# Kernel tuning notes

Measured on AMD Instinct MI355X. Metric: run time of the kernel, lower is better.

Reference implementation:

```python
import jax, jax.numpy as jnp
import numpy as np

NC = 1
LAMBDA_BOX = 0.05
LAMBDA_OBJ = 1.0
LAMBDA_CLS = 0.5

# yolov5s pixel-space anchors (already stride-scaled): [n_scales=3, A=3, 2]
_ANCHORS = np.array([[[10, 13], [16, 30], [33, 23]],
                     [[30, 61], [62, 45], [59, 119]],
                     [[116, 90], [156, 198], [373, 326]]], dtype=np.float32)

B, N = 64, 32
GRIDS = [160, 80, 40]  # 1280px input, strides 8/16/32


def setup_inputs() -> dict:
    key = jax.random.key(0)
    k0, k1, k2, kb = jax.random.split(key, 4)
    A = _ANCHORS.shape[1]
    preds = {}
    for i, (k, g) in enumerate(zip((k0, k1, k2), GRIDS)):
        preds[f"pred{i}"] = jax.random.normal(k, (B, A * (NC + 5), g, g), dtype=jnp.float32)
    # normalized cxcywh boxes, kept strictly inside (0,1) so gi<W, gj<H and w,h>0
    boxes = jax.random.uniform(kb, (B, N, 4), minval=0.02, maxval=0.98, dtype=jnp.float32)
    labels = jnp.zeros((B, N), dtype=jnp.int32)  # nc=1 -> all class 0
    scaled_anchors = jnp.asarray(_ANCHORS)
    return {**preds, "boxes": boxes, "labels": labels, "scaled_anchors": scaled_anchors}


def _scale_loss(pred, boxes, anchor_grid, nc):
    # pred: [B, A*(nc+5), H, W]; boxes: [B, N, 4] normalized cxcywh; anchor_grid: [A, 2]
    Bc, _, H, W = pred.shape
    A = anchor_grid.shape[0]
    Nc = boxes.shape[1]
    p = pred.reshape(Bc, A, nc + 5, H, W).transpose(0, 1, 3, 4, 2)  # [B,A,H,W,nc+5]

    scale = jnp.array([W, H, W, H], dtype=pred.dtype)
    bx = boxes * scale                                   # grid-space cxcywh [B,N,4]
    gx, gy, gw, gh = bx[..., 0], bx[..., 1], bx[..., 2], bx[..., 3]
    gi = gx.astype(jnp.int32)                            # int() truncation (boxes > 0)
    gj = gy.astype(jnp.int32)

    # anchor matching: min(ratio, 1/ratio) product, argmax over A
    r = anchor_grid[None, None, :, :] / bx[..., None, 2:4]   # [B,N,A,2]
    ious = jnp.minimum(r, 1.0 / r).prod(-1)                  # [B,N,A]
    best = jnp.argmax(ious, axis=-1)                         # [B,N]

    bi = jnp.broadcast_to(jnp.arange(Bc)[:, None], (Bc, Nc))
    idx = (bi, best, gj, gi)
    aw = anchor_grid[best, 0]
    ah = anchor_grid[best, 1]

    z = jnp.zeros((Bc, A, H, W), dtype=pred.dtype)
    obj = jnp.zeros((Bc, A, H, W), dtype=bool).at[idx].set(True)
    tx = z.at[idx].set(gx - gi.astype(pred.dtype))
    ty = z.at[idx].set(gy - gj.astype(pred.dtype))
    tw = z.at[idx].set(jnp.log(gw / aw + 1e-16))
    th = z.at[idx].set(jnp.log(gh / ah + 1e-16))

    objf = obj.astype(pred.dtype)
    n_pos = objf.sum()
    n_neg = (1.0 - objf).sum()

    # sum of 4 per-component MSE means == combined squared-error sum / n_pos
    sq = ((p[..., 0] - tx) ** 2 + (p[..., 1] - ty) ** 2
          + (p[..., 2] - tw) ** 2 + (p[..., 3] - th) ** 2)
    loss_box = (sq * objf).sum() / n_pos

    po = p[..., 4]
    # BCEWithLogits: target 1 -> softplus(-x); target 0 -> softplus(x)
    loss_obj = ((jax.nn.softplus(-po) * objf).sum() / n_pos
                + (jax.nn.softplus(po) * (1.0 - objf)).sum() / n_neg)
    return loss_box, loss_obj


def reference(pred0, pred1, pred2, boxes, labels, scaled_anchors):
    del labels  # nc == 1 -> original skips the classification loss
    loss_box = 0.0
    loss_obj = 0.0
    for i, pred in enumerate((pred0, pred1, pred2)):
        lb, lo = _scale_loss(pred, boxes, scaled_anchors[i], NC)
        loss_box = loss_box + lb
        loss_obj = loss_obj + lo
    return LAMBDA_BOX * loss_box + LAMBDA_OBJ * loss_obj
```

## Files before the change

kernel.cpp:

```cpp
#include <hip/hip_runtime.h>
#include <math.h>

#define NSCALES 3
#define BATCH 64
#define NBOX 32

#define CELLS0 4915200
#define CELLS1 1228800
#define CELLS2 307200

#define NB0 1200
#define NB1 300
#define NB2 75

struct Accum {
    double box_sum[3];
    double pos_sum[3];
    double neg_corr[3];
    double neg_total[3];
    int n_pos[3];
    int pad;
};

__device__ __forceinline__ float softplusf(float x) {
    return fmaxf(x, 0.0f) + log1pf(expf(-fabsf(x)));
}

__global__ __launch_bounds__(64) void targets_kernel(
    const float* __restrict__ pred0, const float* __restrict__ pred1,
    const float* __restrict__ pred2, const float* __restrict__ boxes,
    const float* __restrict__ anchors, Accum* __restrict__ acc)
{
    const int bs = blockIdx.x;
    const int s  = bs / BATCH;
    const int b  = bs % BATCH;
    const int G  = (s == 0) ? 160 : (s == 1 ? 80 : 40);
    const float* __restrict__ pred = (s == 0) ? pred0 : (s == 1 ? pred1 : pred2);
    const int HW = G * G;
    const int t  = threadIdx.x;

    __shared__ int keys[NBOX];

    float sq = 0.0f, posv = 0.0f, negc = 0.0f;
    int cnt = 0;

    int key = -1;
    float gx = 0.f, gy = 0.f, gw = 1.f, gh = 1.f;
    int gi = 0, gj = 0, best = 0;

    if (t < NBOX) {
        const float4 bx = ((const float4*)boxes)[b * NBOX + t];
        const float fG = (float)G;
        gx = bx.x * fG; gy = bx.y * fG; gw = bx.z * fG; gh = bx.w * fG;
        float bestm = -1.0f;
        #pragma unroll
        for (int a = 0; a < 3; ++a) {
            float aw = anchors[s * 6 + a * 2 + 0];
            float ah = anchors[s * 6 + a * 2 + 1];
            float rw = aw / gw, rh = ah / gh;
            float m = fminf(rw, 1.0f / rw) * fminf(rh, 1.0f / rh);
            if (m > bestm) { bestm = m; best = a; }
        }
        gi = (int)gx;
        gj = (int)gy;
        key = (best * G + gj) * G + gi;
        keys[t] = key;
    }
    __syncthreads();

    if (t < NBOX) {
        bool winner = true;
        for (int u = t + 1; u < NBOX; ++u)
            if (keys[u] == key) winner = false;
        if (winner) {
            float aw = anchors[s * 6 + best * 2 + 0];
            float ah = anchors[s * 6 + best * 2 + 1];
            float tx = gx - (float)gi;
            float ty = gy - (float)gj;
            float tw = logf(gw / aw + 1e-16f);
            float th = logf(gh / ah + 1e-16f);
            size_t base = (size_t)((b * 3 + best) * 6) * (size_t)HW + (size_t)(gj * G + gi);
            float px = pred[base + (size_t)0 * HW];
            float py = pred[base + (size_t)1 * HW];
            float pw = pred[base + (size_t)2 * HW];
            float ph = pred[base + (size_t)3 * HW];
            float po = pred[base + (size_t)4 * HW];
            float dx = px - tx, dy = py - ty, dw = pw - tw, dh = ph - th;
            sq   = dx * dx + dy * dy + dw * dw + dh * dh;
            posv = softplusf(-po);
            negc = softplusf(po);
            cnt  = 1;
        }
    }

    #pragma unroll
    for (int off = 32; off; off >>= 1) {
        sq   += __shfl_down(sq, off);
        posv += __shfl_down(posv, off);
        negc += __shfl_down(negc, off);
        cnt  += __shfl_down(cnt, off);
    }
    if (t == 0) {
        atomicAdd(&acc->box_sum[s],  (double)sq);
        atomicAdd(&acc->pos_sum[s],  (double)posv);
        atomicAdd(&acc->neg_corr[s], (double)negc);
        atomicAdd(&acc->n_pos[s],    cnt);
    }
}

__global__ __launch_bounds__(256) void obj_kernel(
    const float4* __restrict__ p0, const float4* __restrict__ p1,
    const float4* __restrict__ p2, Accum* __restrict__ acc)
{
    const int blk = blockIdx.x;
    int s, HW4, base4;
    const float4* __restrict__ p;
    if (blk < NB0)            { s = 0; p = p0; HW4 = 6400; base4 = blk * 1024; }
    else if (blk < NB0 + NB1) { s = 1; p = p1; HW4 = 1600; base4 = (blk - NB0) * 1024; }
    else                      { s = 2; p = p2; HW4 = 400;  base4 = (blk - NB0 - NB1) * 1024; }

    float sum = 0.0f;
    #pragma unroll
    for (int k = 0; k < 4; ++k) {
        int i4    = base4 + k * 256 + threadIdx.x;
        int plane = i4 / HW4;
        int off4  = i4 - plane * HW4;
        float4 v  = p[(size_t)(plane * 6 + 4) * HW4 + off4];
        sum += softplusf(v.x) + softplusf(v.y) + softplusf(v.z) + softplusf(v.w);
    }

    #pragma unroll
    for (int off = 32; off; off >>= 1) sum += __shfl_down(sum, off);
    __shared__ float wsum[4];
    const int wave = threadIdx.x >> 6;
    if ((threadIdx.x & 63) == 0) wsum[wave] = sum;
    __syncthreads();
    if (threadIdx.x == 0) {
        float tot = wsum[0] + wsum[1] + wsum[2] + wsum[3];
        atomicAdd(&acc->neg_total[s], (double)tot);
    }
}

__global__ void finalize_kernel(const Accum* __restrict__ acc, float* __restrict__ out)
{
    if (threadIdx.x == 0 && blockIdx.x == 0) {
        const double cells[3] = {(double)CELLS0, (double)CELLS1, (double)CELLS2};
        double lb = 0.0, lo = 0.0;
        #pragma unroll
        for (int s = 0; s < 3; ++s) {
            double npos = (double)acc->n_pos[s];
            double nneg = cells[s] - npos;
            lb += acc->box_sum[s] / npos;
            lo += acc->pos_sum[s] / npos
                + (acc->neg_total[s] - acc->neg_corr[s]) / nneg;
        }
        out[0] = (float)(0.05 * lb + 1.0 * lo);
    }
}

extern "C" void kernel_launch(void* const* d_in, const int* in_sizes, int n_in,
                              void* d_out, int out_size, void* d_ws, size_t ws_size,
                              hipStream_t stream) {
    const float* p0      = (const float*)d_in[0];
    const float* p1      = (const float*)d_in[1];
    const float* p2      = (const float*)d_in[2];
    const float* boxes   = (const float*)d_in[3];
    const float* anchors = (const float*)d_in[5];

    Accum* acc = (Accum*)d_ws;
    hipMemsetAsync(d_ws, 0, sizeof(Accum), stream);

    targets_kernel<<<NSCALES * BATCH, 64, 0, stream>>>(p0, p1, p2, boxes, anchors, acc);
    obj_kernel<<<NB0 + NB1 + NB2, 256, 0, stream>>>(
        (const float4*)p0, (const float4*)p1, (const float4*)p2, acc);
    finalize_kernel<<<1, 64, 0, stream>>>(acc, (float*)d_out);
}
```

Baseline: 201.3 us.

## Fuse target and objectness kernels, replace atomics with per-block partials

```diff
diff --git a/kernel.cpp b/kernel.cpp
--- a/kernel.cpp
+++ b/kernel.cpp
@@ -1,58 +1,70 @@
 #include <hip/hip_runtime.h>
 #include <math.h>
-
-#define NSCALES 3
-#define BATCH 64
-#define NBOX 32
-
-#define CELLS0 4915200
-#define CELLS1 1228800
-#define CELLS2 307200
 
 #define NB0 1200
 #define NB1 300
 #define NB2 75
+#define NOBJ (NB0 + NB1 + NB2)
+#define NPAIR 192
+#define NTGT (NPAIR / 8)
+#define CELLS0 4915200.0
+#define CELLS1 1228800.0
+#define CELLS2 307200.0
 
-struct Accum {
-    double box_sum[3];
-    double pos_sum[3];
-    double neg_corr[3];
-    double neg_total[3];
-    int n_pos[3];
-    int pad;
-};
+struct TgtPart { double box, pos, negc, cnt; };
 
 __device__ __forceinline__ float softplusf(float x) {
     return fmaxf(x, 0.0f) + log1pf(expf(-fabsf(x)));
 }
 
-__global__ __launch_bounds__(64) void targets_kernel(
-    const float* __restrict__ pred0, const float* __restrict__ pred1,
-    const float* __restrict__ pred2, const float* __restrict__ boxes,
-    const float* __restrict__ anchors, Accum* __restrict__ acc)
+__global__ __launch_bounds__(256) void main_kernel(
+    const float* __restrict__ p0, const float* __restrict__ p1,
+    const float* __restrict__ p2, const float* __restrict__ boxes,
+    const float* __restrict__ anchors,
+    double* __restrict__ obj_part,
+    TgtPart* __restrict__ tgt_part)
 {
-    const int bs = blockIdx.x;
-    const int s  = bs / BATCH;
-    const int b  = bs % BATCH;
-    const int G  = (s == 0) ? 160 : (s == 1 ? 80 : 40);
-    const float* __restrict__ pred = (s == 0) ? pred0 : (s == 1 ? pred1 : pred2);
-    const int HW = G * G;
-    const int t  = threadIdx.x;
+    const int blk = blockIdx.x;
+    const int tid = threadIdx.x;
 
-    __shared__ int keys[NBOX];
+    if (blk < NOBJ) {
+        int HW4, base4;
+        const float4* __restrict__ p;
+        if (blk < NB0)            { p = (const float4*)p0; HW4 = 6400; base4 = blk * 1024; }
+        else if (blk < NB0 + NB1) { p = (const float4*)p1; HW4 = 1600; base4 = (blk - NB0) * 1024; }
+        else                      { p = (const float4*)p2; HW4 = 400;  base4 = (blk - NB0 - NB1) * 1024; }
 
-    float sq = 0.0f, posv = 0.0f, negc = 0.0f;
-    int cnt = 0;
+        float sum = 0.0f;
+        #pragma unroll
+        for (int k = 0; k < 4; ++k) {
+            int i4    = base4 + k * 256 + tid;
+            int plane = i4 / HW4;
+            int off4  = i4 - plane * HW4;
+            float4 v  = p[(size_t)(plane * 6 + 4) * HW4 + off4];
+            sum += softplusf(v.x) + softplusf(v.y) + softplusf(v.z) + softplusf(v.w);
+        }
+        #pragma unroll
+        for (int off = 32; off; off >>= 1) sum += __shfl_down(sum, off);
+        __shared__ float wsum[4];
+        if ((tid & 63) == 0) wsum[tid >> 6] = sum;
+        __syncthreads();
+        if (tid == 0)
+            obj_part[blk] = (double)(wsum[0] + wsum[1] + wsum[2] + wsum[3]);
+    } else {
+        const int g  = tid >> 5, l = tid & 31;
+        const int pi = (blk - NOBJ) * 8 + g;
+        const int s  = pi >> 6, b = pi & 63;
+        const int G  = (s == 0) ? 160 : (s == 1 ? 80 : 40);
+        const float* __restrict__ pred = (s == 0) ? p0 : (s == 1 ? p1 : p2);
+        const int HW = G * G;
 
-    int key = -1;
-    float gx = 0.f, gy = 0.f, gw = 1.f, gh = 1.f;
-    int gi = 0, gj = 0, best = 0;
+        __shared__ int keys[8][32];
 
-    if (t < NBOX) {
-        const float4 bx = ((const float4*)boxes)[b * NBOX + t];
+        const float4 bx = ((const float4*)boxes)[b * 32 + l];
         const float fG = (float)G;
-        gx = bx.x * fG; gy = bx.y * fG; gw = bx.z * fG; gh = bx.w * fG;
-        float bestm = -1.0f;
+        const float gx = bx.x * fG, gy = bx.y * fG, gw = bx.z * fG, gh = bx.w * fG;
+
+        int best = 0; float bestm = -1.0f;
         #pragma unroll
         for (int a = 0; a < 3; ++a) {
             float aw = anchors[s * 6 + a * 2 + 0];
@@ -61,24 +73,20 @@
             float m = fminf(rw, 1.0f / rw) * fminf(rh, 1.0f / rh);
             if (m > bestm) { bestm = m; best = a; }
         }
-        gi = (int)gx;
-        gj = (int)gy;
-        key = (best * G + gj) * G + gi;
-        keys[t] = key;
-    }
-    __syncthreads();
+        const int gi = (int)gx, gj = (int)gy;
+        const int key = (best * G + gj) * G + gi;
+        keys[g][l] = key;
+        __syncthreads();
 
-    if (t < NBOX) {
+        float sq = 0.0f, posv = 0.0f, negc = 0.0f; int cnt = 0;
         bool winner = true;
-        for (int u = t + 1; u < NBOX; ++u)
-            if (keys[u] == key) winner = false;
+        for (int u = l + 1; u < 32; ++u)
+            if (keys[g][u] == key) winner = false;
         if (winner) {
             float aw = anchors[s * 6 + best * 2 + 0];
             float ah = anchors[s * 6 + best * 2 + 1];
-            float tx = gx - (float)gi;
-            float ty = gy - (float)gj;
-            float tw = logf(gw / aw + 1e-16f);
-            float th = logf(gh / ah + 1e-16f);
+            float tx = gx - (float)gi, ty = gy - (float)gj;
+            float tw = logf(gw / aw + 1e-16f), th = logf(gh / ah + 1e-16f);
             size_t base = (size_t)((b * 3 + best) * 6) * (size_t)HW + (size_t)(gj * G + gi);
             float px = pred[base + (size_t)0 * HW];
             float py = pred[base + (size_t)1 * HW];
@@ -91,68 +99,72 @@
             negc = softplusf(po);
             cnt  = 1;
         }
-    }
 
-    #pragma unroll
-    for (int off = 32; off; off >>= 1) {
-        sq   += __shfl_down(sq, off);
-        posv += __shfl_down(posv, off);
-        negc += __shfl_down(negc, off);
-        cnt  += __shfl_down(cnt, off);
-    }
-    if (t == 0) {
-        atomicAdd(&acc->box_sum[s],  (double)sq);
-        atomicAdd(&acc->pos_sum[s],  (double)posv);
-        atomicAdd(&acc->neg_corr[s], (double)negc);
-        atomicAdd(&acc->n_pos[s],    cnt);
+        float fcnt = (float)cnt;
+        #pragma unroll
+        for (int off = 16; off; off >>= 1) {
+            sq   += __shfl_down(sq,   off, 32);
+            posv += __shfl_down(posv, off, 32);
+            negc += __shfl_down(negc, off, 32);
+            fcnt += __shfl_down(fcnt, off, 32);
+        }
+        if (l == 0) {
+            TgtPart t; t.box = sq; t.pos = posv; t.negc = negc; t.cnt = fcnt;
+            tgt_part[pi] = t;
+        }
     }
 }
 
-__global__ __launch_bounds__(256) void obj_kernel(
-    const float4* __restrict__ p0, const float4* __restrict__ p1,
-    const float4* __restrict__ p2, Accum* __restrict__ acc)
+__global__ __launch_bounds__(256) void finalize_kernel(
+    const double* __restrict__ obj_part, const TgtPart* __restrict__ tgt_part,
+    float* __restrict__ out)
 {
-    const int blk = blockIdx.x;
-    int s, HW4, base4;
-    const float4* __restrict__ p;
-    if (blk < NB0)            { s = 0; p = p0; HW4 = 6400; base4 = blk * 1024; }
-    else if (blk < NB0 + NB1) { s = 1; p = p1; HW4 = 1600; base4 = (blk - NB0) * 1024; }
-    else                      { s = 2; p = p2; HW4 = 400;  base4 = (blk - NB0 - NB1) * 1024; }
+    __shared__ double negtot_s[3], box_s[3], pos_s[3], negc_s[3], cnt_s[3];
+    const int tid = threadIdx.x;
+    const int wave = tid >> 6, lane = tid & 63;
 
-    float sum = 0.0f;
-    #pragma unroll
-    for (int k = 0; k < 4; ++k) {
-        int i4    = base4 + k * 256 + threadIdx.x;
-        int plane = i4 / HW4;
-        int off4  = i4 - plane * HW4;
-        float4 v  = p[(size_t)(plane * 6 + 4) * HW4 + off4];
-        sum += softplusf(v.x) + softplusf(v.y) + softplusf(v.z) + softplusf(v.w);
+    if (wave < 3) {
+        const int start = (wave == 0) ? 0   : (wave == 1 ? NB0       : NB0 + NB1);
+        const int end   = (wave == 0) ? NB0 : (wave == 1 ? NB0 + NB1 : NOBJ);
+        double sum = 0.0;
+        for (int i = start + lane; i < end; i += 64) sum += obj_part[i];
+        #pragma unroll
+        for (int off = 32; off; off >>= 1) sum += __shfl_down(sum, off);
+        if (lane == 0) negtot_s[wave] = sum;
+    } else {
+        double bx[3], ps[3], ng[3], ct[3];
+        #pragma unroll
+        for (int q = 0; q < 3; ++q) {
+            TgtPart t = tgt_part[lane + 64 * q];
+            bx[q] = t.box; ps[q] = t.pos; ng[q] = t.negc; ct[q] = t.cnt;
+        }
+        #pragma unroll
+        for (int off = 32; off; off >>= 1) {
+            #pragma unroll
+            for (int q = 0; q < 3; ++q) {
+                bx[q] += __shfl_down(bx[q], off);
+                ps[q] += __shfl_down(ps[q], off);
+                ng[q] += __shfl_down(ng[q], off);
+                ct[q] += __shfl_down(ct[q], off);
+            }
+        }
+        if (lane == 0) {
+            #pragma unroll
+            for (int q = 0; q < 3; ++q) {
+                box_s[q] = bx[q]; pos_s[q] = ps[q]; negc_s[q] = ng[q]; cnt_s[q] = ct[q];
+            }
+        }
     }
-
-    #pragma unroll
-    for (int off = 32; off; off >>= 1) sum += __shfl_down(sum, off);
-    __shared__ float wsum[4];
-    const int wave = threadIdx.x >> 6;
-    if ((threadIdx.x & 63) == 0) wsum[wave] = sum;
     __syncthreads();
-    if (threadIdx.x == 0) {
-        float tot = wsum[0] + wsum[1] + wsum[2] + wsum[3];
-        atomicAdd(&acc->neg_total[s], (double)tot);
-    }
-}
-
-__global__ void finalize_kernel(const Accum* __restrict__ acc, float* __restrict__ out)
-{
-    if (threadIdx.x == 0 && blockIdx.x == 0) {
-        const double cells[3] = {(double)CELLS0, (double)CELLS1, (double)CELLS2};
+    if (tid == 0) {
+        const double cells[3] = {CELLS0, CELLS1, CELLS2};
         double lb = 0.0, lo = 0.0;
         #pragma unroll
         for (int s = 0; s < 3; ++s) {
-            double npos = (double)acc->n_pos[s];
+            double npos = cnt_s[s];
             double nneg = cells[s] - npos;
-            lb += acc->box_sum[s] / npos;
-            lo += acc->pos_sum[s] / npos
-                + (acc->neg_total[s] - acc->neg_corr[s]) / nneg;
+            lb += box_s[s] / npos;
+            lo += pos_s[s] / npos + (negtot_s[s] - negc_s[s]) / nneg;
         }
         out[0] = (float)(0.05 * lb + 1.0 * lo);
     }
@@ -167,11 +179,10 @@
     const float* boxes   = (const float*)d_in[3];
     const float* anchors = (const float*)d_in[5];
 
-    Accum* acc = (Accum*)d_ws;
-    hipMemsetAsync(d_ws, 0, sizeof(Accum), stream);
+    double*  obj_part = (double*)d_ws;
+    TgtPart* tgt_part = (TgtPart*)((char*)d_ws + NOBJ * sizeof(double));
 
-    targets_kernel<<<NSCALES * BATCH, 64, 0, stream>>>(p0, p1, p2, boxes, anchors, acc);
-    obj_kernel<<<NB0 + NB1 + NB2, 256, 0, stream>>>(
-        (const float4*)p0, (const float4*)p1, (const float4*)p2, acc);
-    finalize_kernel<<<1, 64, 0, stream>>>(acc, (float*)d_out);
+    main_kernel<<<NOBJ + NTGT, 256, 0, stream>>>(p0, p1, p2, boxes, anchors,
+                                                 obj_part, tgt_part);
+    finalize_kernel<<<1, 256, 0, stream>>>(obj_part, tgt_part, (float*)d_out);
 }
```

Result: faster. 191.8 us (median of 2 runs) (-4.7%).
